# Performance work log

Measured on AMD Instinct MI355X. Metric: run time of the kernel, lower is better.

The kernel has to match this reference:

```python
import jax, jax.numpy as jnp
import numpy as np

B, S, HID, NH = 4, 2048, 512, 8
DH = HID // NH
NEG = -1000000.0


def setup_inputs() -> dict:
    key = jax.random.key(0)
    ks = jax.random.split(key, 8)
    scale = 1.0 / np.sqrt(HID)
    return {
        "queries": jax.random.normal(ks[0], (B, S, HID), dtype=jnp.float32),
        "keys": jax.random.normal(ks[1], (B, S, HID), dtype=jnp.float32),
        "values": jax.random.normal(ks[2], (B, S, HID), dtype=jnp.float32),
        "valid_lens": jax.random.randint(ks[3], (B,), 1, S + 1, dtype=jnp.int32),
        "Wq": jax.random.uniform(ks[4], (HID, HID), jnp.float32, -scale, scale),
        "Wk": jax.random.uniform(ks[5], (HID, HID), jnp.float32, -scale, scale),
        "Wv": jax.random.uniform(ks[6], (HID, HID), jnp.float32, -scale, scale),
        "Wo": jax.random.uniform(ks[7], (HID, HID), jnp.float32, -scale, scale),
    }


def _split_heads(x):
    # (B, S, HID) -> (B, NH, S, DH)
    return x.reshape(B, S, NH, DH).transpose(0, 2, 1, 3)


def reference(queries, keys, values, valid_lens, Wq, Wk, Wv, Wo):
    q = _split_heads(queries @ Wq.T)
    k = _split_heads(keys @ Wk.T)
    v = _split_heads(values @ Wv.T)
    scores = jnp.einsum("bhqd,bhkd->bhqk", q, k) / jnp.sqrt(jnp.float32(DH))
    # valid_lens is per-batch; mask key positions >= valid_len with -1e6 (as in sequence_mask)
    mask = jnp.arange(S)[None, :] < valid_lens[:, None]          # (B, S)
    scores = jnp.where(mask[:, None, None, :], scores, NEG)
    attn = jax.nn.softmax(scores, axis=-1)
    out = jnp.einsum("bhqk,bhkd->bhqd", attn, v)                 # (B, NH, S, DH)
    out = out.transpose(0, 2, 1, 3).reshape(B, S, HID)
    return out @ Wo.T
```

## Files before the change

kernel.cpp:

```cpp
#include <hip/hip_runtime.h>

#define B_ 4
#define S_ 2048
#define HIDN 512
#define NH 8
#define DH 64

typedef __attribute__((ext_vector_type(8))) short short8;
typedef __attribute__((ext_vector_type(4))) short short4v;
typedef __attribute__((ext_vector_type(8))) __bf16 bf16x8;
typedef __attribute__((ext_vector_type(4))) float floatx4;
typedef __attribute__((ext_vector_type(2))) unsigned uint2v;
typedef __attribute__((ext_vector_type(4))) unsigned uint4v;

__device__ inline short f2bf(float f) {
    union { float f; unsigned u; } x; x.f = f;
    unsigned r = x.u + 0x7fffu + ((x.u >> 16) & 1u);
    return (short)(r >> 16);
}

__device__ inline unsigned pack2(float a, float b) {
    unsigned ua = __builtin_bit_cast(unsigned, a) + 0x8000u;
    unsigned ub = __builtin_bit_cast(unsigned, b) + 0x8000u;
    return __builtin_amdgcn_perm(ub, ua, 0x07060302);
}

__device__ inline unsigned cvtpk2(float a, float b) {
    unsigned r;
    asm("v_cvt_pk_bf16_f32 %0, %1, %2" : "=v"(r) : "v"(a), "v"(b));
    return r;
}

__device__ inline short8 cvt8(const float* __restrict__ p) {
    floatx4 f0 = *(const floatx4*)p;
    floatx4 f1 = *(const floatx4*)(p + 4);
    uint4v u;
    u[0] = pack2(f0[0], f0[1]); u[1] = pack2(f0[2], f0[3]);
    u[2] = pack2(f1[0], f1[1]); u[3] = pack2(f1[2], f1[3]);
    return __builtin_bit_cast(short8, u);
}

__device__ inline floatx4 mfma_s(short8 a, short8 b, floatx4 c) {
    return __builtin_amdgcn_mfma_f32_16x16x32_bf16(
        __builtin_bit_cast(bf16x8, a), __builtin_bit_cast(bf16x8, b), c, 0, 0, 0);
}

__global__ __launch_bounds__(256) void gemm_qkv(const float* __restrict__ xq,
                                                const float* __restrict__ xk,
                                                const float* __restrict__ xv,
                                                const float* __restrict__ wqf,
                                                const float* __restrict__ wkf,
                                                const float* __restrict__ wvf,
                                                const int* __restrict__ vlen,
                                                short* __restrict__ Qh,
                                                short* __restrict__ Kh,
                                                short* __restrict__ VT) {
    const int fid = blockIdx.x;
    const int xh = fid & 7;
    const int g  = fid >> 3;
    const int xl = g / 12;
    const int rrp = g - xl * 12;
    const int y  = rrp / 3;
    const int z  = rrp - y * 3;
    const int x  = xh * 8 + xl;

    const float* X = z == 0 ? xq : (z == 1 ? xk : xv);
    const float* W = z == 0 ? wqf : (z == 1 ? wkf : wvf);
    short* dstQK = z == 0 ? Qh : Kh;

    const int t = threadIdx.x;
    const int m0 = x * 128, n0 = y * 128;
    const int bb = m0 >> 11, sbase = m0 & 2047;

    if (z >= 1) {
        const int vl = vlen[bb];
        if (sbase >= vl) {
            if (z == 2) {
#pragma unroll
                for (int p = 0; p < 8; p++) {
                    int idx = p * 256 + t;
                    int nn = idx >> 4;
                    int ch = idx & 15;
                    int n = n0 + nn;
                    int h = n >> 6, d = n & 63;
                    short8 zz = {0,0,0,0,0,0,0,0};
                    *(short8*)&VT[((bb * NH + h) * DH + d) * S_ + sbase + ch * 8] = zz;
                }
            }
            return;
        }
    }

    __shared__ __align__(16) short smem[128 * 72 * 2];
    short (*Als)[72] = (short(*)[72])smem;
    short (*Bls)[72] = (short(*)[72])(smem + 128 * 72);
    short* Cls = smem;

    const int w = t >> 6, lane = t & 63, quad = lane >> 4, l16 = lane & 15;
    const int wm = (w & 1) * 64, wn = (w >> 1) * 64;

    floatx4 acc[4][4];
    floatx4 zero = {0.f, 0.f, 0.f, 0.f};
#pragma unroll
    for (int i = 0; i < 4; i++)
#pragma unroll
        for (int j = 0; j < 4; j++) acc[i][j] = zero;

    const int row0 = t >> 3;
    const int c8 = (t & 7) * 8;

    for (int k0 = 0; k0 < HIDN; k0 += 64) {
        __syncthreads();
#pragma unroll
        for (int rr = 0; rr < 4; rr++)
            *(short8*)&Als[row0 + rr*32][c8] =
                cvt8(&X[(m0 + row0 + rr*32) * HIDN + k0 + c8]);
#pragma unroll
        for (int rr = 0; rr < 4; rr++)
            *(short8*)&Bls[row0 + rr*32][c8] =
                cvt8(&W[(n0 + row0 + rr*32) * HIDN + k0 + c8]);
        __syncthreads();

#pragma unroll
        for (int ks = 0; ks < 2; ks++) {
            const int cq8 = (ks * 4 + quad) * 8;
            short8 a[4], b[4];
#pragma unroll
            for (int i = 0; i < 4; i++)
                a[i] = *(const short8*)&Als[wm + i*16 + l16][cq8];
#pragma unroll
            for (int j = 0; j < 4; j++)
                b[j] = *(const short8*)&Bls[wn + j*16 + l16][cq8];
#pragma unroll
            for (int i = 0; i < 4; i++)
#pragma unroll
                for (int j = 0; j < 4; j++)
                    acc[i][j] = mfma_s(a[i], b[j], acc[i][j]);
        }
    }

    __syncthreads();
    if (z < 2) {
#pragma unroll
        for (int i = 0; i < 4; i++)
#pragma unroll
            for (int j = 0; j < 4; j++) {
                int n_l = wn + j*16 + l16;
#pragma unroll
                for (int r = 0; r < 4; r++) {
                    int m_l = wm + i*16 + quad*4 + r;
                    Cls[m_l * 136 + n_l] = f2bf(acc[i][j][r]);
                }
            }
        __syncthreads();
#pragma unroll
        for (int p = 0; p < 8; p++) {
            int idx = p * 256 + t;
            int mr = idx >> 4;
            int ch = idx & 15;
            short8 v = *(const short8*)&Cls[mr * 136 + ch * 8];
            int n = n0 + ch * 8;
            int h = n >> 6, d = n & 63;
            *(short8*)&dstQK[((bb * NH + h) * S_ + sbase + mr) * DH + d] = v;
        }
    } else {
#pragma unroll
        for (int i = 0; i < 4; i++)
#pragma unroll
            for (int j = 0; j < 4; j++) {
                int n_l = wn + j*16 + l16;
                int m_l = wm + i*16 + quad*4;
                uint2v pv;
                pv[0] = pack2(acc[i][j][0], acc[i][j][1]);
                pv[1] = pack2(acc[i][j][2], acc[i][j][3]);
                *(uint2v*)&Cls[n_l * 136 + m_l] = pv;
            }
        __syncthreads();
#pragma unroll
        for (int p = 0; p < 8; p++) {
            int idx = p * 256 + t;
            int nn = idx >> 4;
            int ch = idx & 15;
            short8 v = *(const short8*)&Cls[nn * 136 + ch * 8];
            int n = n0 + nn;
            int h = n >> 6, d = n & 63;
            *(short8*)&VT[((bb * NH + h) * DH + d) * S_ + sbase + ch * 8] = v;
        }
    }
}

__global__ __launch_bounds__(256) void gemm_out(const short* __restrict__ AO,
                                                const float* __restrict__ Wo,
                                                float* __restrict__ C) {
    const int fid = blockIdx.x;
    const int xh = fid & 7;
    const int g  = fid >> 3;
    const int xl = g >> 3;
    const int y  = g & 7;
    const int x  = xh * 8 + xl;

    __shared__ __align__(16) short Als[128][72];
    __shared__ __align__(16) short Bls[64][72];

    const int t = threadIdx.x;
    const int w = t >> 6, lane = t & 63, quad = lane >> 4, l16 = lane & 15;
    const int wm = (w & 1) * 64, wn = (w >> 1) * 32;
    const int m0 = x * 128, n0 = y * 64;

    floatx4 acc[4][2];
    floatx4 zero = {0.f, 0.f, 0.f, 0.f};
#pragma unroll
    for (int i = 0; i < 4; i++)
#pragma unroll
        for (int j = 0; j < 2; j++) acc[i][j] = zero;

    const int row0 = t >> 3;
    const int c8 = (t & 7) * 8;

    for (int k0 = 0; k0 < HIDN; k0 += 64) {
        __syncthreads();
#pragma unroll
        for (int rr = 0; rr < 4; rr++)
            *(short8*)&Als[row0 + rr*32][c8] =
                *(const short8*)&AO[(m0 + row0 + rr*32) * HIDN + k0 + c8];
#pragma unroll
        for (int rr = 0; rr < 2; rr++)
            *(short8*)&Bls[row0 + rr*32][c8] =
                cvt8(&Wo[(n0 + row0 + rr*32) * HIDN + k0 + c8]);
        __syncthreads();

#pragma unroll
        for (int ks = 0; ks < 2; ks++) {
            const int cq8 = (ks * 4 + quad) * 8;
            short8 a[4], b[2];
#pragma unroll
            for (int i = 0; i < 4; i++)
                a[i] = *(const short8*)&Als[wm + i*16 + l16][cq8];
#pragma unroll
            for (int j = 0; j < 2; j++)
                b[j] = *(const short8*)&Bls[wn + j*16 + l16][cq8];
#pragma unroll
            for (int i = 0; i < 4; i++)
#pragma unroll
                for (int j = 0; j < 2; j++)
                    acc[i][j] = mfma_s(a[i], b[j], acc[i][j]);
        }
    }

#pragma unroll
    for (int i = 0; i < 4; i++)
#pragma unroll
        for (int j = 0; j < 2; j++)
#pragma unroll
            for (int r = 0; r < 4; r++) {
                int m = m0 + wm + i*16 + quad*4 + r;
                int n = n0 + wn + j*16 + l16;
                C[m * HIDN + n] = acc[i][j][r];
            }
}

__global__ __launch_bounds__(256, 4) void attn_kernel(const short* __restrict__ Qh,
                                                      const short* __restrict__ Kh,
                                                      const short* __restrict__ VT,
                                                      const int* __restrict__ vlen,
                                                      short* __restrict__ AO) {
    __shared__ __align__(16) short Ksh[128 * 64];
    __shared__ __align__(16) short Vsh[64 * 128];
    short* Psh = Ksh;

    const int t = threadIdx.x, w = t >> 6, lane = t & 63;
    const int quad = lane >> 4, l16 = lane & 15;

    const int orig = blockIdx.x;
    const int wgid = ((orig & 7) << 7) + (orig >> 3);
    const int h = wgid >> 7;
    const int rem = wgid & 127;
    const int b = rem >> 5;
    const int qb = (rem & 31) * 64;
    const int bh = b * NH + h;
    const int vl = vlen[b];
    const int nfull = vl >> 7, rem128 = vl & 127;
    const int nt = nfull + (rem128 ? 1 : 0);

    const float SC = 0.180336879f;

    const short* qrow = &Qh[(bh * S_ + qb + w * 16 + l16) * DH];
    short8 qa0 = *(const short8*)&qrow[quad * 8];
    short8 qa1 = *(const short8*)&qrow[32 + quad * 8];

    const short ONE = (short)0x3F80;
    short8 ones = {ONE, ONE, ONE, ONE, ONE, ONE, ONE, ONE};

    floatx4 Oacc[4];
    floatx4 Lacc;
    floatx4 zero = {0.f, 0.f, 0.f, 0.f};
#pragma unroll
    for (int dt = 0; dt < 4; dt++) Oacc[dt] = zero;
    Lacc = zero;

    for (int kt = 0; kt < nt; kt++) {
        const int base = kt << 7;
        const bool bnd = (base + 128) > vl;
        __syncthreads();
        {
            const short* Kg = &Kh[(bh * S_ + base) * DH];
#pragma unroll
            for (int it = 0; it < 4; it++) {
                int idx = it * 256 + t;
                int row = idx >> 3, c = idx & 7;
                *(short8*)&Ksh[row * 64 + (((c ^ (row & 7))) << 3)] =
                    *(const short8*)&Kg[row * DH + (c << 3)];
            }
            const short* Vg = &VT[bh * DH * S_ + base];
#pragma unroll
            for (int it = 0; it < 4; it++) {
                int idx = it * 256 + t;
                int d = idx >> 4, c = idx & 15;
                *(short8*)&Vsh[d * 128 + (((c ^ (d & 7))) << 3)] =
                    *(const short8*)&Vg[d * S_ + (c << 3)];
            }
        }
        __syncthreads();

        floatx4 sc[8];
        __builtin_amdgcn_s_setprio(1);
#pragma unroll
        for (int n = 0; n < 8; n++) {
            int krow = n * 16 + l16;
            const short* kr = &Ksh[krow * 64];
            short8 kb0 = *(const short8*)&kr[((quad ^ (krow & 7)) << 3)];
            short8 kb1 = *(const short8*)&kr[(((4 + quad) ^ (krow & 7)) << 3)];
            floatx4 s = zero;
            s = mfma_s(kb0, qa0, s);
            s = mfma_s(kb1, qa1, s);
            sc[n] = s;
        }
        __builtin_amdgcn_s_setprio(0);
        __syncthreads();

        if (bnd) {
#pragma unroll
            for (int n = 0; n < 8; n++)
#pragma unroll
                for (int r = 0; r < 4; r++) {
                    int key = base + n * 16 + quad * 4 + r;
                    if (key >= vl) sc[n][r] = -1e30f;
                }
        }
#pragma unroll
        for (int n = 0; n < 8; n++)
#pragma unroll
            for (int r = 0; r < 4; r++)
                sc[n][r] = __builtin_amdgcn_exp2f(sc[n][r] * SC);

#pragma unroll
        for (int n = 0; n < 8; n++) {
            int c = (n << 1) + (quad >> 1);
            int idx = (w << 11) + (l16 << 7) + ((c ^ (l16 & 7)) << 3) + ((quad & 1) << 2);
            uint2v pv;
            pv[0] = cvtpk2(sc[n][0], sc[n][1]);
            pv[1] = cvtpk2(sc[n][2], sc[n][3]);
            *(uint2v*)&Psh[idx] = pv;
        }
        asm volatile("s_waitcnt lgkmcnt(0)" ::: "memory");
        __builtin_amdgcn_sched_barrier(0);

        __builtin_amdgcn_s_setprio(1);
#pragma unroll
        for (int kk = 0; kk < 4; kk++) {
            int pc = (kk << 2) + quad;
            short8 pf = *(const short8*)&Psh[(w << 11) + (l16 << 7) + ((pc ^ (l16 & 7)) << 3)];
            Lacc = mfma_s(ones, pf, Lacc);
#pragma unroll
            for (int dt = 0; dt < 4; dt++) {
                int vrow = dt * 16 + l16;
                short8 vf = *(const short8*)&Vsh[vrow * 128 + ((pc ^ (vrow & 7)) << 3)];
                Oacc[dt] = mfma_s(vf, pf, Oacc[dt]);
            }
        }
        __builtin_amdgcn_s_setprio(0);
    }

    float inv = 1.0f / Lacc[0];
    int q = qb + w * 16 + l16;
    short* dst = &AO[(b * S_ + q) * HIDN + h * DH];
#pragma unroll
    for (int dt = 0; dt < 4; dt++) {
        uint2v v;
        v[0] = cvtpk2(Oacc[dt][0] * inv, Oacc[dt][1] * inv);
        v[1] = cvtpk2(Oacc[dt][2] * inv, Oacc[dt][3] * inv);
        *(uint2v*)&dst[dt * 16 + quad * 4] = v;
    }
}

extern "C" void kernel_launch(void* const* d_in, const int* in_sizes, int n_in,
                              void* d_out, int out_size, void* d_ws, size_t ws_size,
                              hipStream_t stream) {
    const float* q  = (const float*)d_in[0];
    const float* k  = (const float*)d_in[1];
    const float* v  = (const float*)d_in[2];
    const int*   vl = (const int*)d_in[3];
    const float* wq = (const float*)d_in[4];
    const float* wk = (const float*)d_in[5];
    const float* wv = (const float*)d_in[6];
    const float* wo = (const float*)d_in[7];
    float* out = (float*)d_out;

    const size_t HSZ = (size_t)B_ * NH * S_ * DH;
    short* Qh  = (short*)d_ws;
    short* Kh  = Qh + HSZ;
    short* VT  = Kh + HSZ;
    short* AO  = VT + HSZ;

    dim3 blk(256);
    gemm_qkv<<<dim3(768), blk, 0, stream>>>(q, k, v, wq, wk, wv, vl, Qh, Kh, VT);
    attn_kernel<<<dim3(1024), blk, 0, stream>>>(Qh, Kh, VT, vl, AO);
    gemm_out<<<dim3(512), blk, 0, stream>>>(AO, wo, out);
}
```

Before: 165.7 us.

## Load K and V fragments directly from global memory, dropping LDS staging

Removes the shared-memory staging of K and V tiles and the block-wide barriers around them. Each wave now reads its MFMA operands for K and V^T straight from global memory (relying on L1/L2 cache reuse across waves), and LDS holds only a per-wave P buffer. This cuts barrier stalls and LDS traffic but makes each of the four waves fetch the same K/V data separately, and the global loads are strided and less coalesced.

```diff
diff --git a/kernel.cpp b/kernel.cpp
--- a/kernel.cpp
+++ b/kernel.cpp
@@ -264,12 +264,11 @@
                                                       const short* __restrict__ VT,
                                                       const int* __restrict__ vlen,
                                                       short* __restrict__ AO) {
-    __shared__ __align__(16) short Ksh[128 * 64];
-    __shared__ __align__(16) short Vsh[64 * 128];
-    short* Psh = Ksh;
+    __shared__ __align__(16) short Pbuf[4 * 2048];
 
     const int t = threadIdx.x, w = t >> 6, lane = t & 63;
     const int quad = lane >> 4, l16 = lane & 15;
+    short* Psh = &Pbuf[w << 11];
 
     const int orig = blockIdx.x;
     const int wgid = ((orig & 7) << 7) + (orig >> 3);
@@ -291,6 +290,9 @@
     const short ONE = (short)0x3F80;
     short8 ones = {ONE, ONE, ONE, ONE, ONE, ONE, ONE, ONE};
 
+    const short* Kgb = &Kh[(size_t)bh * S_ * DH];
+    const short* Vgb = &VT[(size_t)bh * DH * S_];
+
     floatx4 Oacc[4];
     floatx4 Lacc;
     floatx4 zero = {0.f, 0.f, 0.f, 0.f};
@@ -301,42 +303,21 @@
     for (int kt = 0; kt < nt; kt++) {
         const int base = kt << 7;
         const bool bnd = (base + 128) > vl;
-        __syncthreads();
-        {
-            const short* Kg = &Kh[(bh * S_ + base) * DH];
-#pragma unroll
-            for (int it = 0; it < 4; it++) {
-                int idx = it * 256 + t;
-                int row = idx >> 3, c = idx & 7;
-                *(short8*)&Ksh[row * 64 + (((c ^ (row & 7))) << 3)] =
-                    *(const short8*)&Kg[row * DH + (c << 3)];
-            }
-            const short* Vg = &VT[bh * DH * S_ + base];
-#pragma unroll
-            for (int it = 0; it < 4; it++) {
-                int idx = it * 256 + t;
-                int d = idx >> 4, c = idx & 15;
-                *(short8*)&Vsh[d * 128 + (((c ^ (d & 7))) << 3)] =
-                    *(const short8*)&Vg[d * S_ + (c << 3)];
-            }
-        }
-        __syncthreads();
-
+
+        const short* Kg = Kgb + (size_t)base * DH;
         floatx4 sc[8];
         __builtin_amdgcn_s_setprio(1);
 #pragma unroll
         for (int n = 0; n < 8; n++) {
-            int krow = n * 16 + l16;
-            const short* kr = &Ksh[krow * 64];
-            short8 kb0 = *(const short8*)&kr[((quad ^ (krow & 7)) << 3)];
-            short8 kb1 = *(const short8*)&kr[(((4 + quad) ^ (krow & 7)) << 3)];
+            int kro = n * 16 + l16;
+            short8 kb0 = *(const short8*)&Kg[kro * DH + quad * 8];
+            short8 kb1 = *(const short8*)&Kg[kro * DH + 32 + quad * 8];
             floatx4 s = zero;
             s = mfma_s(kb0, qa0, s);
             s = mfma_s(kb1, qa1, s);
             sc[n] = s;
         }
         __builtin_amdgcn_s_setprio(0);
-        __syncthreads();
 
         if (bnd) {
 #pragma unroll
@@ -356,7 +337,7 @@
 #pragma unroll
         for (int n = 0; n < 8; n++) {
             int c = (n << 1) + (quad >> 1);
-            int idx = (w << 11) + (l16 << 7) + ((c ^ (l16 & 7)) << 3) + ((quad & 1) << 2);
+            int idx = (l16 << 7) + ((c ^ (l16 & 7)) << 3) + ((quad & 1) << 2);
             uint2v pv;
             pv[0] = cvtpk2(sc[n][0], sc[n][1]);
             pv[1] = cvtpk2(sc[n][2], sc[n][3]);
@@ -369,12 +350,12 @@
 #pragma unroll
         for (int kk = 0; kk < 4; kk++) {
             int pc = (kk << 2) + quad;
-            short8 pf = *(const short8*)&Psh[(w << 11) + (l16 << 7) + ((pc ^ (l16 & 7)) << 3)];
+            short8 pf = *(const short8*)&Psh[(l16 << 7) + ((pc ^ (l16 & 7)) << 3)];
             Lacc = mfma_s(ones, pf, Lacc);
 #pragma unroll
             for (int dt = 0; dt < 4; dt++) {
                 int vrow = dt * 16 + l16;
-                short8 vf = *(const short8*)&Vsh[vrow * 128 + ((pc ^ (vrow & 7)) << 3)];
+                short8 vf = *(const short8*)&Vgb[(size_t)vrow * S_ + base + pc * 8];
                 Oacc[dt] = mfma_s(vf, pf, Oacc[dt]);
             }
         }
```

Measured after the change: 259.5 us. 1.57x slower.
